# Kernel optimization log

Hardware: AMD Instinct MI355X
Metric: run time of the kernel (lower is better)

The kernel has to match this reference:

```python
import jax, jax.numpy as jnp
import numpy as np

N = 50000        # num nodes
IN = 128         # in_features
H = 4            # num heads
C = 32           # out features per head (out_features // num_heads, concat_heads=True)
E_RAND = 450000  # random edges (plus N self-loops -> E = 500000)
ALPHA = 0.2      # LeakyReLU negative slope


def setup_inputs() -> dict:
    key = jax.random.key(0)
    k1, k2, k3, k4 = jax.random.split(key, 4)
    x = jax.random.normal(k1, (N, IN), jnp.float32)
    # xavier_uniform-ish scale with gain 1.414 (std = gain*sqrt(2/(fan_in+fan_out)))
    W = jax.random.normal(k2, (H * C, IN), jnp.float32) * (1.414 * np.sqrt(2.0 / (IN + H * C)))
    b = jnp.zeros((H * C,), jnp.float32)
    a = jax.random.normal(k3, (H, 2 * C), jnp.float32) * (1.414 * np.sqrt(2.0 / (H + 2 * C)))
    # self-loops guarantee every source node has >=1 edge, so the edge-wise
    # segment softmax matches the dense masked softmax of the original module.
    self_loops = jnp.stack([jnp.arange(N, dtype=jnp.int32)] * 2, axis=1)
    rand_edges = jax.random.randint(k4, (E_RAND, 2), 0, N, jnp.int32)
    edges = jnp.concatenate([self_loops, rand_edges], axis=0)  # (E, 2) = (src, dst)
    return {"x": x, "W": W, "b": b, "a": a, "edges": edges}


def reference(x, W, b, a, edges):
    num_nodes = x.shape[0]
    # projection: (N, IN) -> (N, H, C)
    h = (x @ W.T + b).reshape(num_nodes, H, C)
    src, dst = edges[:, 0], edges[:, 1]
    hs = h[src]  # (E, H, C) gather of source node feats
    hd = h[dst]  # (E, H, C) gather of destination node feats
    a_input = jnp.concatenate([hs, hd], axis=-1)  # (E, H, 2C)
    logits = jnp.einsum('ehc,hc->eh', a_input, a)
    logits = jax.nn.leaky_relu(logits, ALPHA)
    # segment softmax over outgoing edges of each source node (== dense masked
    # softmax over dim=2 in the original, given every node has >=1 out-edge)
    m = jax.lax.stop_gradient(jax.ops.segment_max(logits, src, num_segments=num_nodes))
    ex = jnp.exp(logits - m[src])
    denom = jax.ops.segment_sum(ex, src, num_segments=num_nodes)
    probs = ex / denom[src]  # (E, H)
    # weighted scatter-aggregate of destination feats into source nodes
    out = jax.ops.segment_sum(probs[..., None] * hd, src, num_segments=num_nodes)  # (N, H, C)
    return out.reshape(1, num_nodes, H * C)  # concat_heads=True, batch_size=1
```

## Files before the change

### kernel.cpp

```cpp
#include <hip/hip_runtime.h>
#include <math.h>

#define LRELU_ALPHA 0.2f
#define CAP 64

typedef __attribute__((ext_vector_type(8))) short bf16x8;
typedef __attribute__((ext_vector_type(4))) float f32x4;

__device__ __forceinline__ void split2(float f0, float f1, unsigned& hi, unsigned& lo) {
    unsigned u0 = __float_as_uint(f0), u1 = __float_as_uint(f1);
    unsigned h0 = u0 & 0xFFFF0000u, h1 = u1 & 0xFFFF0000u;
    float l0f = f0 - __uint_as_float(h0);
    float l1f = f1 - __uint_as_float(h1);
    hi = (h0 >> 16) | h1;
    lo = (__float_as_uint(l0f) >> 16) | (__float_as_uint(l1f) & 0xFFFF0000u);
}
__device__ __forceinline__ unsigned short f2bf(float f) {
    unsigned u = __float_as_uint(f);
    return (unsigned short)((u + 0x7FFFu + ((u >> 16) & 1u)) >> 16);
}
__device__ __forceinline__ float bf2f(unsigned short s) {
    return __uint_as_float(((unsigned)s) << 16);
}

__global__ __launch_bounds__(256) void k_init(const float* __restrict__ W,
                                              bf16x8* __restrict__ wf,
                                              int* __restrict__ cnt, int N) {
    int i = blockIdx.x * 256 + threadIdx.x;
    if (i < N) cnt[i] = 0;
    if (blockIdx.x < 8) {
        int id = i;
        int lane = id & 63, ks = (id >> 6) & 3, ct = id >> 8;
        int j = ct * 16 + (lane & 15);
        int k0 = ks * 32 + ((lane >> 4) << 3);
        const float* wp = W + j * 128 + k0;
        float4 f0 = *reinterpret_cast<const float4*>(wp);
        float4 f1 = *reinterpret_cast<const float4*>(wp + 4);
        uint4 hv, lv;
        split2(f0.x, f0.y, hv.x, lv.x);
        split2(f0.z, f0.w, hv.y, lv.y);
        split2(f1.x, f1.y, hv.z, lv.z);
        split2(f1.z, f1.w, hv.w, lv.w);
        *reinterpret_cast<uint4*>(&wf[id]) = hv;
        *reinterpret_cast<uint4*>(&wf[2048 + id]) = lv;
    }
}

__global__ __launch_bounds__(256) void k_gemm(const float* __restrict__ x,
                                              const bf16x8* __restrict__ wf,
                                              const float* __restrict__ b,
                                              const float* __restrict__ a,
                                              unsigned short* __restrict__ hb,
                                              float* __restrict__ asrc,
                                              float* __restrict__ adst, int N,
                                              const int* __restrict__ edges,
                                              int* __restrict__ cnt,
                                              unsigned short* __restrict__ col, int E) {
    __shared__ __align__(16) unsigned char sXH[32 * 256];
    __shared__ __align__(16) unsigned char sXL[32 * 256];
    const int t = threadIdx.x;
    const int w = t >> 6;
    const int l = t & 63;
    const int base = blockIdx.x * 32;

    for (int e = blockIdx.x * 256 + t; e < E; e += gridDim.x * 256) {
        int2 ed = *reinterpret_cast<const int2*>(&edges[(size_t)e * 2]);
        int pos = atomicAdd(&cnt[ed.x], 1);
        if (pos < CAP) col[ed.x * CAP + pos] = (unsigned short)ed.y;
    }

    bf16x8 wh[2][4], wl[2][4];
    #pragma unroll
    for (int ctl = 0; ctl < 2; ++ctl)
        #pragma unroll
        for (int ks = 0; ks < 4; ++ks) {
            int fid = (((2 * w + ctl) * 4 + ks) << 6) + l;
            wh[ctl][ks] = wf[fid];
            wl[ctl][ks] = wf[2048 + fid];
        }

    int jj[2];
    float bv[2], asw[2], adw[2];
    #pragma unroll
    for (int ctl = 0; ctl < 2; ++ctl) {
        jj[ctl] = w * 32 + ctl * 16 + (l & 15);
        bv[ctl] = b[jj[ctl]];
        asw[ctl] = a[w * 64 + ctl * 16 + (l & 15)];
        adw[ctl] = a[w * 64 + 32 + ctl * 16 + (l & 15)];
    }

    #pragma unroll
    for (int i = 0; i < 4; ++i) {
        int f = t + i * 256;
        int r = f >> 5, c4 = f & 31;
        int gr = base + r;
        float4 v = (gr < N) ? *reinterpret_cast<const float4*>(x + (size_t)gr * 128 + c4 * 4)
                            : make_float4(0.f, 0.f, 0.f, 0.f);
        unsigned h01, h23, l01, l23;
        split2(v.x, v.y, h01, l01);
        split2(v.z, v.w, h23, l23);
        int boff = r * 256 + ((c4 * 8) ^ ((r & 7) << 4));
        *reinterpret_cast<uint2*>(sXH + boff) = make_uint2(h01, h23);
        *reinterpret_cast<uint2*>(sXL + boff) = make_uint2(l01, l23);
    }
    __syncthreads();

    f32x4 acc[2][2];
    #pragma unroll
    for (int rt = 0; rt < 2; ++rt)
        #pragma unroll
        for (int ctl = 0; ctl < 2; ++ctl)
            acc[rt][ctl] = (f32x4){0.f, 0.f, 0.f, 0.f};

    #pragma unroll
    for (int ks = 0; ks < 4; ++ks) {
        #pragma unroll
        for (int rt = 0; rt < 2; ++rt) {
            int r = rt * 16 + (l & 15);
            int boff = r * 256 + (((ks * 64) + ((l >> 4) << 4)) ^ ((r & 7) << 4));
            bf16x8 xh = *reinterpret_cast<const bf16x8*>(sXH + boff);
            bf16x8 xl = *reinterpret_cast<const bf16x8*>(sXL + boff);
            #pragma unroll
            for (int ctl = 0; ctl < 2; ++ctl) {
                acc[rt][ctl] = __builtin_amdgcn_mfma_f32_16x16x32_bf16(xh, wh[ctl][ks], acc[rt][ctl], 0, 0, 0);
                acc[rt][ctl] = __builtin_amdgcn_mfma_f32_16x16x32_bf16(xh, wl[ctl][ks], acc[rt][ctl], 0, 0, 0);
                acc[rt][ctl] = __builtin_amdgcn_mfma_f32_16x16x32_bf16(xl, wh[ctl][ks], acc[rt][ctl], 0, 0, 0);
            }
        }
    }

    #pragma unroll
    for (int rt = 0; rt < 2; ++rt) {
        #pragma unroll
        for (int reg = 0; reg < 4; ++reg) {
            int n = base + rt * 16 + ((l >> 4) << 2) + reg;
            bool ok = (n < N);
            float v0 = acc[rt][0][reg] + bv[0];
            float v1 = acc[rt][1][reg] + bv[1];
            float ps = v0 * asw[0] + v1 * asw[1];
            float pd = v0 * adw[0] + v1 * adw[1];
            #pragma unroll
            for (int mask = 1; mask <= 8; mask <<= 1) {
                ps += __shfl_xor(ps, mask);
                pd += __shfl_xor(pd, mask);
            }
            if (ok && (l & 15) == 0) {
                asrc[n * 4 + w] = ps;
                adst[n * 4 + w] = pd;
            }
        }
    }

    __syncthreads();
    unsigned short* sH = reinterpret_cast<unsigned short*>(sXH);
    #pragma unroll
    for (int rt = 0; rt < 2; ++rt) {
        #pragma unroll
        for (int reg = 0; reg < 4; ++reg) {
            int r = rt * 16 + ((l >> 4) << 2) + reg;
            sH[r * 128 + jj[0]] = f2bf(acc[rt][0][reg] + bv[0]);
            sH[r * 128 + jj[1]] = f2bf(acc[rt][1][reg] + bv[1]);
        }
    }
    __syncthreads();
    {
        int row = t >> 3;
        int off = (t & 7) * 16;
        int n = base + row;
        if (n < N) {
            const uint4* sp = reinterpret_cast<const uint4*>(sH + row * 128 + off);
            uint4* dp = reinterpret_cast<uint4*>(hb + (size_t)n * 128 + off);
            dp[0] = sp[0];
            dp[1] = sp[1];
        }
    }
}

__global__ __launch_bounds__(256) void k_node(const int* __restrict__ cnt,
                                              const unsigned short* __restrict__ col,
                                              const float* __restrict__ asrc,
                                              const float* __restrict__ adst,
                                              const unsigned short* __restrict__ hb,
                                              float* __restrict__ out, int N) {
    int n = blockIdx.x * 8 + (threadIdx.x >> 5);
    if (n >= N) return;
    int l = threadIdx.x & 31;
    int hd = l >> 3;
    float asr = asrc[n * 4 + hd];
    int deg = min(cnt[n], CAP);
    const unsigned short* cp = col + n * CAP;
    float ax = 0.f, ay = 0.f, az = 0.f, aw = 0.f, den = 0.f;
    int c0 = cp[0];
    int kmax = (deg + 7) & ~7;
    for (int k = 0; k < kmax; k += 8) {
        uint4 cw = *reinterpret_cast<const uint4*>(cp + k);
        int c[8] = {(int)(cw.x & 0xFFFFu), (int)(cw.x >> 16),
                    (int)(cw.y & 0xFFFFu), (int)(cw.y >> 16),
                    (int)(cw.z & 0xFFFFu), (int)(cw.z >> 16),
                    (int)(cw.w & 0xFFFFu), (int)(cw.w >> 16)};
        float ev[8];
        #pragma unroll
        for (int u = 0; u < 8; ++u) {
            bool okk = (k + u) < deg;
            c[u] = okk ? c[u] : c0;
            float g = asr + adst[c[u] * 4 + hd];
            g = (g >= 0.f) ? g : LRELU_ALPHA * g;
            ev[u] = okk ? __expf(g) : 0.f;
        }
        #pragma unroll
        for (int u = 0; u < 8; ++u) {
            ushort4 q = *reinterpret_cast<const ushort4*>(&hb[(size_t)c[u] * 128 + l * 4]);
            ax += ev[u] * bf2f(q.x); ay += ev[u] * bf2f(q.y);
            az += ev[u] * bf2f(q.z); aw += ev[u] * bf2f(q.w);
            den += ev[u];
        }
    }
    float inv = 1.f / den;
    f32x4 o = (f32x4){ax * inv, ay * inv, az * inv, aw * inv};
    __builtin_nontemporal_store(o, reinterpret_cast<f32x4*>(&out[(size_t)n * 128 + l * 4]));
}

extern "C" void kernel_launch(void* const* d_in, const int* in_sizes, int n_in,
                              void* d_out, int out_size, void* d_ws, size_t ws_size,
                              hipStream_t stream) {
    const float* x = (const float*)d_in[0];
    const float* W = (const float*)d_in[1];
    const float* b = (const float*)d_in[2];
    const float* a = (const float*)d_in[3];
    const int* edges = (const int*)d_in[4];
    const int N = in_sizes[0] / 128;
    const int E = in_sizes[4] / 2;
    float* out = (float*)d_out;

    char* ws = (char*)d_ws;
    unsigned short* hb = (unsigned short*)ws; ws += (size_t)N * 128 * 2;
    float* asrc = (float*)ws;     ws += (size_t)N * 4 * 4;
    float* adst = (float*)ws;     ws += (size_t)N * 4 * 4;
    int* cnt = (int*)ws;          ws += (size_t)N * 4;
    unsigned short* col = (unsigned short*)ws; ws += (size_t)N * CAP * 2;
    bf16x8* wf = (bf16x8*)ws;     ws += (size_t)4096 * 16;

    const int nb = (N + 255) / 256;
    hipLaunchKernelGGL(k_init, dim3(nb), dim3(256), 0, stream, W, wf, cnt, N);
    hipLaunchKernelGGL(k_gemm, dim3((N + 31) / 32), dim3(256), 0, stream,
                       x, wf, b, a, hb, asrc, adst, N, edges, cnt, col, E);
    hipLaunchKernelGGL(k_node, dim3((N + 7) / 8), dim3(256), 0, stream,
                       cnt, col, asrc, adst, hb, out, N);
}
```

Baseline: 76.53 us.

## Process two 32-row tiles per GEMM block with prefetch of second tile

The projection kernel now handles 64 rows per block in two 32-row sub-tiles. The second tile's x rows are loaded into registers before the first tile's MFMAs run, then split and stored to a separate shared-memory region, overlapping global load latency with compute. This halves the grid size, amortizing the weight-fragment register loads and the edge-bucketing setup over more rows. In exchange it uses more registers and 32KB of shared memory, and has fewer blocks to fill the GPU.

```diff
diff --git a/kernel.cpp b/kernel.cpp
--- a/kernel.cpp
+++ b/kernel.cpp
@@ -56,12 +56,11 @@
                                               const int* __restrict__ edges,
                                               int* __restrict__ cnt,
                                               unsigned short* __restrict__ col, int E) {
-    __shared__ __align__(16) unsigned char sXH[32 * 256];
-    __shared__ __align__(16) unsigned char sXL[32 * 256];
+    __shared__ __align__(16) unsigned char sB[32768];
     const int t = threadIdx.x;
     const int w = t >> 6;
     const int l = t & 63;
-    const int base = blockIdx.x * 32;
+    const int base = blockIdx.x * 64;
 
     for (int e = blockIdx.x * 256 + t; e < E; e += gridDim.x * 256) {
         int2 ed = *reinterpret_cast<const int2*>(&edges[(size_t)e * 2]);
@@ -89,6 +88,7 @@
         adw[ctl] = a[w * 64 + 32 + ctl * 16 + (l & 15)];
     }
 
+    const int fr = t >> 5;
     #pragma unroll
     for (int i = 0; i < 4; ++i) {
         int f = t + i * 256;
@@ -100,17 +100,30 @@
         split2(v.x, v.y, h01, l01);
         split2(v.z, v.w, h23, l23);
         int boff = r * 256 + ((c4 * 8) ^ ((r & 7) << 4));
-        *reinterpret_cast<uint2*>(sXH + boff) = make_uint2(h01, h23);
-        *reinterpret_cast<uint2*>(sXL + boff) = make_uint2(l01, l23);
+        *reinterpret_cast<uint2*>(sB + boff) = make_uint2(h01, h23);
+        *reinterpret_cast<uint2*>(sB + 8192 + boff) = make_uint2(l01, l23);
+    }
+    (void)fr;
+
+    float4 ld1[4];
+    #pragma unroll
+    for (int i = 0; i < 4; ++i) {
+        int f = t + i * 256;
+        int r = f >> 5, c4 = f & 31;
+        int gr = base + 32 + r;
+        ld1[i] = (gr < N) ? *reinterpret_cast<const float4*>(x + (size_t)gr * 128 + c4 * 4)
+                          : make_float4(0.f, 0.f, 0.f, 0.f);
     }
     __syncthreads();
 
-    f32x4 acc[2][2];
-    #pragma unroll
-    for (int rt = 0; rt < 2; ++rt)
-        #pragma unroll
-        for (int ctl = 0; ctl < 2; ++ctl)
-            acc[rt][ctl] = (f32x4){0.f, 0.f, 0.f, 0.f};
+    f32x4 acc[2][2][2];
+    #pragma unroll
+    for (int ti = 0; ti < 2; ++ti)
+        #pragma unroll
+        for (int rt = 0; rt < 2; ++rt)
+            #pragma unroll
+            for (int ctl = 0; ctl < 2; ++ctl)
+                acc[ti][rt][ctl] = (f32x4){0.f, 0.f, 0.f, 0.f};
 
     #pragma unroll
     for (int ks = 0; ks < 4; ++ks) {
@@ -118,60 +131,92 @@
         for (int rt = 0; rt < 2; ++rt) {
             int r = rt * 16 + (l & 15);
             int boff = r * 256 + (((ks * 64) + ((l >> 4) << 4)) ^ ((r & 7) << 4));
-            bf16x8 xh = *reinterpret_cast<const bf16x8*>(sXH + boff);
-            bf16x8 xl = *reinterpret_cast<const bf16x8*>(sXL + boff);
+            bf16x8 xh = *reinterpret_cast<const bf16x8*>(sB + boff);
+            bf16x8 xl = *reinterpret_cast<const bf16x8*>(sB + 8192 + boff);
             #pragma unroll
             for (int ctl = 0; ctl < 2; ++ctl) {
-                acc[rt][ctl] = __builtin_amdgcn_mfma_f32_16x16x32_bf16(xh, wh[ctl][ks], acc[rt][ctl], 0, 0, 0);
-                acc[rt][ctl] = __builtin_amdgcn_mfma_f32_16x16x32_bf16(xh, wl[ctl][ks], acc[rt][ctl], 0, 0, 0);
-                acc[rt][ctl] = __builtin_amdgcn_mfma_f32_16x16x32_bf16(xl, wh[ctl][ks], acc[rt][ctl], 0, 0, 0);
-            }
-        }
-    }
-
-    #pragma unroll
-    for (int rt = 0; rt < 2; ++rt) {
-        #pragma unroll
-        for (int reg = 0; reg < 4; ++reg) {
-            int n = base + rt * 16 + ((l >> 4) << 2) + reg;
-            bool ok = (n < N);
-            float v0 = acc[rt][0][reg] + bv[0];
-            float v1 = acc[rt][1][reg] + bv[1];
-            float ps = v0 * asw[0] + v1 * asw[1];
-            float pd = v0 * adw[0] + v1 * adw[1];
-            #pragma unroll
-            for (int mask = 1; mask <= 8; mask <<= 1) {
-                ps += __shfl_xor(ps, mask);
-                pd += __shfl_xor(pd, mask);
-            }
-            if (ok && (l & 15) == 0) {
-                asrc[n * 4 + w] = ps;
-                adst[n * 4 + w] = pd;
-            }
-        }
-    }
-
+                acc[0][rt][ctl] = __builtin_amdgcn_mfma_f32_16x16x32_bf16(xh, wh[ctl][ks], acc[0][rt][ctl], 0, 0, 0);
+                acc[0][rt][ctl] = __builtin_amdgcn_mfma_f32_16x16x32_bf16(xh, wl[ctl][ks], acc[0][rt][ctl], 0, 0, 0);
+                acc[0][rt][ctl] = __builtin_amdgcn_mfma_f32_16x16x32_bf16(xl, wh[ctl][ks], acc[0][rt][ctl], 0, 0, 0);
+            }
+        }
+    }
+
+    #pragma unroll
+    for (int i = 0; i < 4; ++i) {
+        int f = t + i * 256;
+        int r = f >> 5, c4 = f & 31;
+        unsigned h01, h23, l01, l23;
+        split2(ld1[i].x, ld1[i].y, h01, l01);
+        split2(ld1[i].z, ld1[i].w, h23, l23);
+        int boff = r * 256 + ((c4 * 8) ^ ((r & 7) << 4));
+        *reinterpret_cast<uint2*>(sB + 16384 + boff) = make_uint2(h01, h23);
+        *reinterpret_cast<uint2*>(sB + 24576 + boff) = make_uint2(l01, l23);
+    }
     __syncthreads();
-    unsigned short* sH = reinterpret_cast<unsigned short*>(sXH);
-    #pragma unroll
-    for (int rt = 0; rt < 2; ++rt) {
-        #pragma unroll
-        for (int reg = 0; reg < 4; ++reg) {
-            int r = rt * 16 + ((l >> 4) << 2) + reg;
-            sH[r * 128 + jj[0]] = f2bf(acc[rt][0][reg] + bv[0]);
-            sH[r * 128 + jj[1]] = f2bf(acc[rt][1][reg] + bv[1]);
-        }
-    }
+
+    #pragma unroll
+    for (int ks = 0; ks < 4; ++ks) {
+        #pragma unroll
+        for (int rt = 0; rt < 2; ++rt) {
+            int r = rt * 16 + (l & 15);
+            int boff = r * 256 + (((ks * 64) + ((l >> 4) << 4)) ^ ((r & 7) << 4));
+            bf16x8 xh = *reinterpret_cast<const bf16x8*>(sB + 16384 + boff);
+            bf16x8 xl = *reinterpret_cast<const bf16x8*>(sB + 24576 + boff);
+            #pragma unroll
+            for (int ctl = 0; ctl < 2; ++ctl) {
+                acc[1][rt][ctl] = __builtin_amdgcn_mfma_f32_16x16x32_bf16(xh, wh[ctl][ks], acc[1][rt][ctl], 0, 0, 0);
+                acc[1][rt][ctl] = __builtin_amdgcn_mfma_f32_16x16x32_bf16(xh, wl[ctl][ks], acc[1][rt][ctl], 0, 0, 0);
+                acc[1][rt][ctl] = __builtin_amdgcn_mfma_f32_16x16x32_bf16(xl, wh[ctl][ks], acc[1][rt][ctl], 0, 0, 0);
+            }
+        }
+    }
+
+    #pragma unroll
+    for (int ti = 0; ti < 2; ++ti) {
+        #pragma unroll
+        for (int rt = 0; rt < 2; ++rt) {
+            #pragma unroll
+            for (int reg = 0; reg < 4; ++reg) {
+                int n = base + ti * 32 + rt * 16 + ((l >> 4) << 2) + reg;
+                bool ok = (n < N);
+                float v0 = acc[ti][rt][0][reg] + bv[0];
+                float v1 = acc[ti][rt][1][reg] + bv[1];
+                float ps = v0 * asw[0] + v1 * asw[1];
+                float pd = v0 * adw[0] + v1 * adw[1];
+                #pragma unroll
+                for (int mask = 1; mask <= 8; mask <<= 1) {
+                    ps += __shfl_xor(ps, mask);
+                    pd += __shfl_xor(pd, mask);
+                }
+                if (ok && (l & 15) == 0) {
+                    asrc[n * 4 + w] = ps;
+                    adst[n * 4 + w] = pd;
+                }
+            }
+        }
+    }
+
+    unsigned short* sH = reinterpret_cast<unsigned short*>(sB);
+    #pragma unroll
+    for (int ti = 0; ti < 2; ++ti)
+        #pragma unroll
+        for (int rt = 0; rt < 2; ++rt)
+            #pragma unroll
+            for (int reg = 0; reg < 4; ++reg) {
+                int r = ti * 32 + rt * 16 + ((l >> 4) << 2) + reg;
+                sH[r * 128 + jj[0]] = f2bf(acc[ti][rt][0][reg] + bv[0]);
+                sH[r * 128 + jj[1]] = f2bf(acc[ti][rt][1][reg] + bv[1]);
+            }
     __syncthreads();
     {
-        int row = t >> 3;
-        int off = (t & 7) * 16;
+        int row = t >> 2;
+        int off = (t & 3) * 32;
         int n = base + row;
         if (n < N) {
             const uint4* sp = reinterpret_cast<const uint4*>(sH + row * 128 + off);
             uint4* dp = reinterpret_cast<uint4*>(hb + (size_t)n * 128 + off);
-            dp[0] = sp[0];
-            dp[1] = sp[1];
+            dp[0] = sp[0]; dp[1] = sp[1]; dp[2] = sp[2]; dp[3] = sp[3];
         }
     }
 }
@@ -242,7 +287,7 @@
 
     const int nb = (N + 255) / 256;
     hipLaunchKernelGGL(k_init, dim3(nb), dim3(256), 0, stream, W, wf, cnt, N);
-    hipLaunchKernelGGL(k_gemm, dim3((N + 31) / 32), dim3(256), 0, stream,
+    hipLaunchKernelGGL(k_gemm, dim3((N + 63) / 64), dim3(256), 0, stream,
                        x, wf, b, a, hb, asrc, adst, N, edges, cnt, col, E);
     hipLaunchKernelGGL(k_node, dim3((N + 7) / 8), dim3(256), 0, stream,
                        cnt, col, asrc, adst, hb, out, N);
```

After: 94.56 us. +23.6%, slower.
